# Kernel optimization log

Measured on AMD Instinct MI355X. Metric: run time of the kernel, lower is better.

Reference implementation:

```python
import jax, jax.numpy as jnp
import numpy as np

DEPTH = 5

def _gru_step(h, fmess, bgraph, W_z_w, W_z_b, W_r_w, U_r_w, U_r_b, W_h_w, W_h_b):
    # h: [E, H]; gather neighbor states -> [E, K, H]
    h_nei = h[bgraph]
    sum_h = h_nei.sum(axis=1)                                   # [E, H]
    z_in = jnp.concatenate([fmess, sum_h], axis=1)              # [E, I+H]
    z = jax.nn.sigmoid(z_in @ W_z_w.T + W_z_b)                  # [E, H]
    r1 = (fmess @ W_r_w.T)[:, None, :]                          # [E, 1, H]
    r2 = jnp.einsum('ekh,oh->eko', h_nei, U_r_w) + U_r_b        # [E, K, H]
    r = jax.nn.sigmoid(r1 + r2)
    sum_gated_h = (r * h_nei).sum(axis=1)                       # [E, H]
    h_in = jnp.concatenate([fmess, sum_gated_h], axis=1)
    pre_h = jnp.tanh(h_in @ W_h_w.T + W_h_b)
    new_h = (1.0 - z) * sum_h + z * pre_h
    # row 0 is the padding message; zero it each step
    return new_h.at[0, :].set(0.0)


def setup_inputs() -> dict:
    key = jax.random.key(0)
    ks = jax.random.split(key, 8)
    E, K, I, H = 150000, 8, 128, 128
    s = 0.05
    return {
        'fmess': jax.random.normal(ks[0], (E, I), dtype=jnp.float32),
        'bgraph': jax.random.randint(ks[1], (E, K), 0, E, dtype=jnp.int64),
        'W_z_w': jax.random.normal(ks[2], (H, I + H), dtype=jnp.float32) * s,
        'W_z_b': jnp.zeros((H,), dtype=jnp.float32),
        'W_r_w': jax.random.normal(ks[3], (H, I), dtype=jnp.float32) * s,
        'U_r_w': jax.random.normal(ks[4], (H, H), dtype=jnp.float32) * s,
        'U_r_b': jnp.zeros((H,), dtype=jnp.float32),
        'W_h_w': jax.random.normal(ks[5], (H, I + H), dtype=jnp.float32) * s,
        'W_h_b': jnp.zeros((H,), dtype=jnp.float32),
    }


def reference(fmess, bgraph, W_z_w, W_z_b, W_r_w, U_r_w, U_r_b, W_h_w, W_h_b):
    E = fmess.shape[0]
    H = W_z_w.shape[0]
    h = jnp.zeros((E, H), dtype=fmess.dtype)
    for _ in range(DEPTH):
        h = _gru_step(h, fmess, bgraph, W_z_w, W_z_b, W_r_w, U_r_w, U_r_b, W_h_w, W_h_b)
    return h
```

## Files before the change

kernel.cpp:

```cpp
#include <hip/hip_runtime.h>
#include <cstddef>
#include <cstdint>

typedef __attribute__((ext_vector_type(8))) short bf16x8;
typedef __attribute__((ext_vector_type(4))) float f32x4;
typedef __attribute__((ext_vector_type(2))) float f32x2;
typedef unsigned int u32t;
typedef unsigned short u16t;
typedef unsigned char u8t;

__device__ inline u16t f2bf(float f) {
  union { float f; unsigned u; } c; c.f = f;
  return (u16t)((c.u + 0x7FFFu + ((c.u >> 16) & 1u)) >> 16);
}
__device__ inline float ubits(u32t u) { union { u32t u; float f; } c; c.u = u; return c.f; }
__device__ inline float bf2f(u16t u) { return ubits(((u32t)u) << 16); }
__device__ inline float fsig(float x) { return __builtin_amdgcn_rcpf(1.f + __expf(-x)); }
__device__ inline float ftanh(float x) {
  float t = __expf(-2.f * fabsf(x));
  return copysignf((1.f - t) * __builtin_amdgcn_rcpf(1.f + t), x);
}
__device__ inline u32t f32x4_to_fp8(float a, float b, float c, float d) {
  int v = __builtin_amdgcn_cvt_pk_fp8_f32(a, b, 0, false);
  v = __builtin_amdgcn_cvt_pk_fp8_f32(c, d, v, true);
  return (u32t)v;
}

__global__ __launch_bounds__(256) void conv_weights(
    const float* __restrict__ Wz, const float* __restrict__ Wr,
    const float* __restrict__ Ur, const float* __restrict__ Wh,
    short* __restrict__ out)
{
  int i = blockIdx.x * 256 + threadIdx.x;
  if (i >= 6 * 16384) return;
  int mat = i >> 14, idx = i & 16383;
  int o = idx >> 7, c = idx & 127;
  float v = 0.f;
  switch (mat) {
    case 0: v = Wz[o * 256 + c];        break;
    case 1: v = Wz[o * 256 + 128 + c];  break;
    case 2: v = Wr[o * 128 + c];        break;
    case 3: v = Wh[o * 256 + c];        break;
    case 4: v = Wh[o * 256 + 128 + c];  break;
    case 5: v = Ur[o * 128 + c];        break;
  }
  out[i] = (short)f2bf(v);
}

__global__ __launch_bounds__(256) void conv_fmess(const float* __restrict__ src,
                                                  u16t* __restrict__ dst, size_t n8)
{
  size_t i = (size_t)blockIdx.x * 256 + threadIdx.x;
  if (i >= n8) return;
  const float4 a = *reinterpret_cast<const float4*>(src + i * 8);
  const float4 b = *reinterpret_cast<const float4*>(src + i * 8 + 4);
  uint4 o;
  o.x = ((u32t)f2bf(a.y) << 16) | f2bf(a.x);
  o.y = ((u32t)f2bf(a.w) << 16) | f2bf(a.z);
  o.z = ((u32t)f2bf(b.y) << 16) | f2bf(b.x);
  o.w = ((u32t)f2bf(b.w) << 16) | f2bf(b.z);
  *reinterpret_cast<uint4*>(dst + i * 8) = o;
}

__global__ void detect64(const int* __restrict__ bg, int* __restrict__ flag) {
  int t = threadIdx.x;
  int v = bg[2 * t + 1];
  unsigned long long m = __ballot(v == 0);
  if (t == 0) *flag = (m == ~0ull) ? 1 : 0;
}

__global__ __launch_bounds__(256) void compact_bg(const int* __restrict__ bg,
                                                  const int* __restrict__ flag,
                                                  int* __restrict__ bg32, int n)
{
  int i = blockIdx.x * 256 + threadIdx.x;
  if (i < n) bg32[i] = (*flag) ? bg[2 * (size_t)i] : bg[i];
}

#define GLD(H0, H1, H2, H3, P0, P1, P2, P3, q, nbb) { \
  int i0_ = __shfl(idx_all, (hf * 4 + (q)) * 8 + (nbb) + 0); \
  int i1_ = __shfl(idx_all, (hf * 4 + (q)) * 8 + (nbb) + 1); \
  int i2_ = __shfl(idx_all, (hf * 4 + (q)) * 8 + (nbb) + 2); \
  int i3_ = __shfl(idx_all, (hf * 4 + (q)) * 8 + (nbb) + 3); \
  H0 = *reinterpret_cast<const uint2*>(Hin + (size_t)i0_ * 128 + l5 * 4); \
  H1 = *reinterpret_cast<const uint2*>(Hin + (size_t)i1_ * 128 + l5 * 4); \
  H2 = *reinterpret_cast<const uint2*>(Hin + (size_t)i2_ * 128 + l5 * 4); \
  H3 = *reinterpret_cast<const uint2*>(Hin + (size_t)i3_ * 128 + l5 * 4); \
  P0 = *reinterpret_cast<const u32t*>(Pin + (size_t)i0_ * 128 + l5 * 4); \
  P1 = *reinterpret_cast<const u32t*>(Pin + (size_t)i1_ * 128 + l5 * 4); \
  P2 = *reinterpret_cast<const u32t*>(Pin + (size_t)i2_ * 128 + l5 * 4); \
  P3 = *reinterpret_cast<const u32t*>(Pin + (size_t)i3_ * 128 + l5 * 4); \
}

#define PRN(HV, PW) { \
  f32x2 plo_ = __builtin_amdgcn_cvt_pk_f32_fp8((int)(PW), false); \
  f32x2 phi_ = __builtin_amdgcn_cvt_pk_f32_fp8((int)(PW), true); \
  float h0_ = ubits(HV.x << 16), h1_ = ubits(HV.x & 0xffff0000u); \
  float h2_ = ubits(HV.y << 16), h3_ = ubits(HV.y & 0xffff0000u); \
  s0 += h0_; g0 += fsig(r10 + plo_.x) * h0_; \
  s1 += h1_; g1 += fsig(r11 + plo_.y) * h1_; \
  s2 += h2_; g2 += fsig(r12 + phi_.x) * h2_; \
  s3 += h3_; g3 += fsig(r13 + phi_.y) * h3_; \
}

#define PR4(HH0, HH1, HH2, HH3, PP0, PP1, PP2, PP3) \
  PRN(HH0, PP0) PRN(HH1, PP1) PRN(HH2, PP2) PRN(HH3, PP3)

#define INITR(q) { \
  int rl_ = wave * 8 + hf * 4 + (q); \
  uint2 rp_ = *reinterpret_cast<const uint2*>(s_R1 + rl_ * 136 + l5 * 4); \
  r10 = ubits(rp_.x << 16); r11 = ubits(rp_.x & 0xffff0000u); \
  r12 = ubits(rp_.y << 16); r13 = ubits(rp_.y & 0xffff0000u); \
  s0 = s1 = s2 = s3 = 0.f; g0 = g1 = g2 = g3 = 0.f; \
}

#define FINR(q) { \
  int rl_ = wave * 8 + hf * 4 + (q); \
  uint2 sp_, gp_; \
  sp_.x = ((u32t)f2bf(s1) << 16) | f2bf(s0); \
  sp_.y = ((u32t)f2bf(s3) << 16) | f2bf(s2); \
  gp_.x = ((u32t)f2bf(g1) << 16) | f2bf(g0); \
  gp_.y = ((u32t)f2bf(g3) << 16) | f2bf(g2); \
  *reinterpret_cast<uint2*>(s_sb + rl_ * 136 + l5 * 4) = sp_; \
  *reinterpret_cast<uint2*>(s_gb + rl_ * 136 + l5 * 4) = gp_; \
}

template<int MODE>
__global__ __launch_bounds__(512, 4) void step_k(
    const u16t* __restrict__ fmb,
    const int*  __restrict__ bg32,
    const u16t* __restrict__ Hin,
    const u8t*  __restrict__ Pin,
    const short* __restrict__ wbf,
    const float* __restrict__ bz, const float* __restrict__ urb, const float* __restrict__ bh,
    u16t* __restrict__ Hout, u8t* __restrict__ Pout, float* __restrict__ houtf, int E)
{
  __shared__ __align__(16) char smem[52224];
  u16t* s_R1 = (u16t*)smem;
  u16t* s_sb = (u16t*)(smem + 17408);
  u16t* s_gb = (u16t*)(smem + 34816);

  const int tid = threadIdx.x, wave = tid >> 6, lane = tid & 63;
  const int cl = lane & 15, kg = lane >> 4;
  const int l5 = lane & 31, hf = lane >> 5;
  const int base = blockIdx.x * 64;
  const int wrow = (wave & 1) * 32, ncol = (wave >> 1) * 32;

  const short* Wzf = wbf;
  const short* Wzh = wbf + 16384;
  const short* Wr  = wbf + 2 * 16384;
  const short* Whf = wbf + 3 * 16384;
  const short* Whh = wbf + 4 * 16384;
  const short* Ur  = wbf + 5 * 16384;

  bf16x8 af[2][4];
  #pragma unroll
  for (int rt = 0; rt < 2; ++rt) {
    int ar = base + wrow + rt * 16 + cl;
    if (ar >= E) ar = E - 1;
    #pragma unroll
    for (int ks = 0; ks < 4; ++ks)
      af[rt][ks] = *reinterpret_cast<const bf16x8*>(fmb + (size_t)ar * 128 + ks * 32 + kg * 8);
  }

  int idx_all = 0;
  if (MODE != 0) {
    int er = base + wave * 8 + (lane >> 3);
    if (er >= E) er = 0;
    idx_all = bg32[(size_t)er * 8 + (lane & 7)];
  }

  if (MODE != 0) {
    f32x4 racc[2][2];
    #pragma unroll
    for (int rt = 0; rt < 2; ++rt)
      #pragma unroll
      for (int nt = 0; nt < 2; ++nt) racc[rt][nt] = (f32x4){0.f, 0.f, 0.f, 0.f};
    #pragma unroll
    for (int ks = 0; ks < 4; ++ks) {
      #pragma unroll
      for (int nt = 0; nt < 2; ++nt) {
        bf16x8 b = *reinterpret_cast<const bf16x8*>(Wr + (size_t)(ncol + nt * 16 + cl) * 128 + ks * 32 + kg * 8);
        #pragma unroll
        for (int rt = 0; rt < 2; ++rt)
          racc[rt][nt] = __builtin_amdgcn_mfma_f32_16x16x32_bf16(af[rt][ks], b, racc[rt][nt], 0, 0, 0);
      }
    }
    #pragma unroll
    for (int nt = 0; nt < 2; ++nt) {
      int n = ncol + nt * 16 + cl;
      float bias = urb[n];
      #pragma unroll
      for (int rt = 0; rt < 2; ++rt)
        #pragma unroll
        for (int r = 0; r < 4; ++r)
          s_R1[(wrow + rt * 16 + kg * 4 + r) * 136 + n] = f2bf(racc[rt][nt][r] + bias);
    }
    __syncthreads();

    uint2 HA0, HA1, HA2, HA3, HB0, HB1, HB2, HB3;
    u32t  PA0, PA1, PA2, PA3, PB0, PB1, PB2, PB3;
    float s0, s1, s2, s3, g0, g1, g2, g3, r10, r11, r12, r13;

    GLD(HA0, HA1, HA2, HA3, PA0, PA1, PA2, PA3, 0, 0)
    GLD(HB0, HB1, HB2, HB3, PB0, PB1, PB2, PB3, 0, 4)
    INITR(0)
    PR4(HA0, HA1, HA2, HA3, PA0, PA1, PA2, PA3)
    GLD(HA0, HA1, HA2, HA3, PA0, PA1, PA2, PA3, 1, 0)
    PR4(HB0, HB1, HB2, HB3, PB0, PB1, PB2, PB3)
    FINR(0)
    GLD(HB0, HB1, HB2, HB3, PB0, PB1, PB2, PB3, 1, 4)
    INITR(1)
    PR4(HA0, HA1, HA2, HA3, PA0, PA1, PA2, PA3)
    GLD(HA0, HA1, HA2, HA3, PA0, PA1, PA2, PA3, 2, 0)
    PR4(HB0, HB1, HB2, HB3, PB0, PB1, PB2, PB3)
    FINR(1)
    GLD(HB0, HB1, HB2, HB3, PB0, PB1, PB2, PB3, 2, 4)
    INITR(2)
    PR4(HA0, HA1, HA2, HA3, PA0, PA1, PA2, PA3)
    GLD(HA0, HA1, HA2, HA3, PA0, PA1, PA2, PA3, 3, 0)
    PR4(HB0, HB1, HB2, HB3, PB0, PB1, PB2, PB3)
    FINR(2)
    GLD(HB0, HB1, HB2, HB3, PB0, PB1, PB2, PB3, 3, 4)
    INITR(3)
    PR4(HA0, HA1, HA2, HA3, PA0, PA1, PA2, PA3)
    PR4(HB0, HB1, HB2, HB3, PB0, PB1, PB2, PB3)
    FINR(3)
    __syncthreads();
  }

  {
    f32x4 acc[2][2];
    #pragma unroll
    for (int rt = 0; rt < 2; ++rt)
      #pragma unroll
      for (int nt = 0; nt < 2; ++nt) acc[rt][nt] = (f32x4){0.f, 0.f, 0.f, 0.f};
    #pragma unroll
    for (int ks = 0; ks < 4; ++ks) {
      bf16x8 as0, as1;
      if (MODE != 0) {
        as0 = *reinterpret_cast<const bf16x8*>(s_sb + (wrow + cl) * 136 + ks * 32 + kg * 8);
        as1 = *reinterpret_cast<const bf16x8*>(s_sb + (wrow + 16 + cl) * 136 + ks * 32 + kg * 8);
      }
      #pragma unroll
      for (int nt = 0; nt < 2; ++nt) {
        int n = ncol + nt * 16 + cl;
        bf16x8 b1 = *reinterpret_cast<const bf16x8*>(Wzf + (size_t)n * 128 + ks * 32 + kg * 8);
        acc[0][nt] = __builtin_amdgcn_mfma_f32_16x16x32_bf16(af[0][ks], b1, acc[0][nt], 0, 0, 0);
        acc[1][nt] = __builtin_amdgcn_mfma_f32_16x16x32_bf16(af[1][ks], b1, acc[1][nt], 0, 0, 0);
        if (MODE != 0) {
          bf16x8 b2 = *reinterpret_cast<const bf16x8*>(Wzh + (size_t)n * 128 + ks * 32 + kg * 8);
          acc[0][nt] = __builtin_amdgcn_mfma_f32_16x16x32_bf16(as0, b2, acc[0][nt], 0, 0, 0);
          acc[1][nt] = __builtin_amdgcn_mfma_f32_16x16x32_bf16(as1, b2, acc[1][nt], 0, 0, 0);
        }
      }
    }
    #pragma unroll
    for (int nt = 0; nt < 2; ++nt) {
      int n = ncol + nt * 16 + cl;
      float bzv = bz[n];
      #pragma unroll
      for (int rt = 0; rt < 2; ++rt)
        #pragma unroll
        for (int r = 0; r < 4; ++r)
          s_R1[(wrow + rt * 16 + kg * 4 + r) * 136 + n] = f2bf(fsig(acc[rt][nt][r] + bzv));
    }
  }

  float nh_sv[2][2][4];
  {
    f32x4 acc[2][2];
    #pragma unroll
    for (int rt = 0; rt < 2; ++rt)
      #pragma unroll
      for (int nt = 0; nt < 2; ++nt) acc[rt][nt] = (f32x4){0.f, 0.f, 0.f, 0.f};
    #pragma unroll
    for (int ks = 0; ks < 4; ++ks) {
      bf16x8 ag0, ag1;
      if (MODE != 0) {
        ag0 = *reinterpret_cast<const bf16x8*>(s_gb + (wrow + cl) * 136 + ks * 32 + kg * 8);
        ag1 = *reinterpret_cast<const bf16x8*>(s_gb + (wrow + 16 + cl) * 136 + ks * 32 + kg * 8);
      }
      #pragma unroll
      for (int nt = 0; nt < 2; ++nt) {
        int n = ncol + nt * 16 + cl;
        bf16x8 b1 = *reinterpret_cast<const bf16x8*>(Whf + (size_t)n * 128 + ks * 32 + kg * 8);
        acc[0][nt] = __builtin_amdgcn_mfma_f32_16x16x32_bf16(af[0][ks], b1, acc[0][nt], 0, 0, 0);
        acc[1][nt] = __builtin_amdgcn_mfma_f32_16x16x32_bf16(af[1][ks], b1, acc[1][nt], 0, 0, 0);
        if (MODE != 0) {
          bf16x8 b2 = *reinterpret_cast<const bf16x8*>(Whh + (size_t)n * 128 + ks * 32 + kg * 8);
          acc[0][nt] = __builtin_amdgcn_mfma_f32_16x16x32_bf16(ag0, b2, acc[0][nt], 0, 0, 0);
          acc[1][nt] = __builtin_amdgcn_mfma_f32_16x16x32_bf16(ag1, b2, acc[1][nt], 0, 0, 0);
        }
      }
    }
    #pragma unroll
    for (int nt = 0; nt < 2; ++nt) {
      int n = ncol + nt * 16 + cl;
      float bhv = bh[n];
      #pragma unroll
      for (int rt = 0; rt < 2; ++rt)
        #pragma unroll
        for (int r = 0; r < 4; ++r) {
          int rowt = wrow + rt * 16 + kg * 4 + r;
          int e = base + rowt;
          float pre = ftanh(acc[rt][nt][r] + bhv);
          float z   = bf2f(s_R1[rowt * 136 + n]);
          float sh  = (MODE == 0) ? 0.f : bf2f(s_sb[rowt * 136 + n]);
          float nh  = (1.f - z) * sh + z * pre;
          if (e == 0) nh = 0.f;
          nh_sv[rt][nt][r] = nh;
        }
    }
  }

  if (MODE == 2) {
    __syncthreads();
    float* so = (float*)(smem + 17408);
    #pragma unroll
    for (int nt = 0; nt < 2; ++nt) {
      int n = ncol + nt * 16 + cl;
      #pragma unroll
      for (int rt = 0; rt < 2; ++rt)
        #pragma unroll
        for (int r = 0; r < 4; ++r)
          so[(wrow + rt * 16 + kg * 4 + r) * 132 + n] = nh_sv[rt][nt][r];
    }
    __syncthreads();
    #pragma unroll
    for (int it = 0; it < 4; ++it) {
      int slot = it * 512 + tid;
      int row = slot >> 5, seg = slot & 31;
      if (base + row < E)
        *reinterpret_cast<float4*>(houtf + (size_t)(base + row) * 128 + seg * 4) =
            *reinterpret_cast<const float4*>(so + row * 132 + seg * 4);
    }
  } else {
    __syncthreads();
    #pragma unroll
    for (int nt = 0; nt < 2; ++nt) {
      int n = ncol + nt * 16 + cl;
      #pragma unroll
      for (int rt = 0; rt < 2; ++rt)
        #pragma unroll
        for (int r = 0; r < 4; ++r)
          s_sb[(wrow + rt * 16 + kg * 4 + r) * 136 + n] = f2bf(nh_sv[rt][nt][r]);
    }
    __syncthreads();
    f32x4 pacc[2][2];
    #pragma unroll
    for (int rt = 0; rt < 2; ++rt)
      #pragma unroll
      for (int nt = 0; nt < 2; ++nt) pacc[rt][nt] = (f32x4){0.f, 0.f, 0.f, 0.f};
    #pragma unroll
    for (int ks = 0; ks < 4; ++ks) {
      bf16x8 ah0 = *reinterpret_cast<const bf16x8*>(s_sb + (wrow + cl) * 136 + ks * 32 + kg * 8);
      bf16x8 ah1 = *reinterpret_cast<const bf16x8*>(s_sb + (wrow + 16 + cl) * 136 + ks * 32 + kg * 8);
      #pragma unroll
      for (int nt = 0; nt < 2; ++nt) {
        bf16x8 b = *reinterpret_cast<const bf16x8*>(Ur + (size_t)(ncol + nt * 16 + cl) * 128 + ks * 32 + kg * 8);
        pacc[0][nt] = __builtin_amdgcn_mfma_f32_16x16x32_bf16(ah0, b, pacc[0][nt], 0, 0, 0);
        pacc[1][nt] = __builtin_amdgcn_mfma_f32_16x16x32_bf16(ah1, b, pacc[1][nt], 0, 0, 0);
      }
    }
    #pragma unroll
    for (int nt = 0; nt < 2; ++nt) {
      int n = ncol + nt * 16 + cl;
      #pragma unroll
      for (int rt = 0; rt < 2; ++rt)
        #pragma unroll
        for (int r = 0; r < 4; ++r)
          s_gb[(wrow + rt * 16 + kg * 4 + r) * 136 + n] = f2bf(pacc[rt][nt][r]);
    }
    __syncthreads();
    #pragma unroll
    for (int it = 0; it < 2; ++it) {
      int slot = it * 512 + tid;
      int row = slot >> 4, seg = slot & 15;
      if (base + row < E)
        *reinterpret_cast<uint4*>(Hout + (size_t)(base + row) * 128 + seg * 8) =
            *reinterpret_cast<const uint4*>(s_sb + row * 136 + seg * 8);
    }
    #pragma unroll
    for (int it = 0; it < 4; ++it) {
      int slot = it * 512 + tid;
      int row = slot >> 5, cg = slot & 31;
      if (base + row < E) {
        uint2 pv = *reinterpret_cast<const uint2*>(s_gb + row * 136 + cg * 4);
        float p0 = ubits(pv.x << 16), p1 = ubits(pv.x & 0xffff0000u);
        float p2 = ubits(pv.y << 16), p3 = ubits(pv.y & 0xffff0000u);
        *reinterpret_cast<u32t*>(Pout + (size_t)(base + row) * 128 + cg * 4) =
            f32x4_to_fp8(p0, p1, p2, p3);
      }
    }
  }
}

extern "C" void kernel_launch(void* const* d_in, const int* in_sizes, int n_in,
                              void* d_out, int out_size, void* d_ws, size_t ws_size,
                              hipStream_t stream) {
  const float* fmess = (const float*)d_in[0];
  const int*   bg    = (const int*)d_in[1];
  const float* Wz    = (const float*)d_in[2];
  const float* bz    = (const float*)d_in[3];
  const float* Wrw   = (const float*)d_in[4];
  const float* Urw   = (const float*)d_in[5];
  const float* urb   = (const float*)d_in[6];
  const float* Wh    = (const float*)d_in[7];
  const float* bh    = (const float*)d_in[8];
  float* out = (float*)d_out;

  const int E = in_sizes[0] / 128;
  const size_t EH = (size_t)E * 128;
  const size_t wshorts = 6 * 16384;

  u16t* HA   = (u16t*)d_ws;
  u8t*  PA   = (u8t*)(HA + EH);
  u16t* fmb  = (u16t*)(PA + EH);
  int*  bg32 = (int*)(fmb + EH);
  short* wbf = (short*)(bg32 + (size_t)E * 8);
  int*  flag = (int*)(wbf + wshorts);
  u16t* HB = (u16t*)d_out;
  u8t*  PB = (u8t*)(HB + EH);

  conv_weights<<<384, 256, 0, stream>>>(Wz, Wrw, Urw, Wh, wbf);
  detect64<<<1, 64, 0, stream>>>(bg, flag);
  compact_bg<<<(E * 8 + 255) / 256, 256, 0, stream>>>(bg, flag, bg32, E * 8);
  conv_fmess<<<(int)((EH / 8 + 255) / 256), 256, 0, stream>>>(fmess, fmb, EH / 8);

  const int grid = (E + 63) / 64;
  step_k<0><<<grid, 512, 0, stream>>>(fmb, bg32, nullptr, nullptr, wbf, bz, urb, bh, HB, PB, nullptr, E);
  step_k<1><<<grid, 512, 0, stream>>>(fmb, bg32, HB, PB, wbf, bz, urb, bh, HA, PA, nullptr, E);
  step_k<1><<<grid, 512, 0, stream>>>(fmb, bg32, HA, PA, wbf, bz, urb, bh, HB, PB, nullptr, E);
  step_k<1><<<grid, 512, 0, stream>>>(fmb, bg32, HB, PB, wbf, bz, urb, bh, HA, PA, nullptr, E);
  step_k<2><<<grid, 512, 0, stream>>>(fmb, bg32, HA, PA, wbf, bz, urb, bh, nullptr, nullptr, out, E);
}
```

Before: 777.2 us.

## Interleave H and P rows into one buffer and shrink shared memory

Stores the bf16 hidden state and the fp8 projected state side by side in a single 384-byte row per edge. Each gathered neighbour then touches one contiguous region instead of two separate arrays. The pre-activation (h) GEMM is moved ahead of the z GEMM, so the tanh result can reuse the gated-sum LDS buffer and z is applied straight from registers. This cuts shared memory from 52KB to 34KB, which may allow more resident blocks, at the cost of an extra barrier.

```diff
diff --git a/kernel.cpp b/kernel.cpp
--- a/kernel.cpp
+++ b/kernel.cpp
@@ -82,14 +82,18 @@
   int i1_ = __shfl(idx_all, (hf * 4 + (q)) * 8 + (nbb) + 1); \
   int i2_ = __shfl(idx_all, (hf * 4 + (q)) * 8 + (nbb) + 2); \
   int i3_ = __shfl(idx_all, (hf * 4 + (q)) * 8 + (nbb) + 3); \
-  H0 = *reinterpret_cast<const uint2*>(Hin + (size_t)i0_ * 128 + l5 * 4); \
-  H1 = *reinterpret_cast<const uint2*>(Hin + (size_t)i1_ * 128 + l5 * 4); \
-  H2 = *reinterpret_cast<const uint2*>(Hin + (size_t)i2_ * 128 + l5 * 4); \
-  H3 = *reinterpret_cast<const uint2*>(Hin + (size_t)i3_ * 128 + l5 * 4); \
-  P0 = *reinterpret_cast<const u32t*>(Pin + (size_t)i0_ * 128 + l5 * 4); \
-  P1 = *reinterpret_cast<const u32t*>(Pin + (size_t)i1_ * 128 + l5 * 4); \
-  P2 = *reinterpret_cast<const u32t*>(Pin + (size_t)i2_ * 128 + l5 * 4); \
-  P3 = *reinterpret_cast<const u32t*>(Pin + (size_t)i3_ * 128 + l5 * 4); \
+  const u16t* r0_ = HPin + (size_t)i0_ * 192; \
+  const u16t* r1_ = HPin + (size_t)i1_ * 192; \
+  const u16t* r2_ = HPin + (size_t)i2_ * 192; \
+  const u16t* r3_ = HPin + (size_t)i3_ * 192; \
+  H0 = *reinterpret_cast<const uint2*>(r0_ + l5 * 4); \
+  H1 = *reinterpret_cast<const uint2*>(r1_ + l5 * 4); \
+  H2 = *reinterpret_cast<const uint2*>(r2_ + l5 * 4); \
+  H3 = *reinterpret_cast<const uint2*>(r3_ + l5 * 4); \
+  P0 = *reinterpret_cast<const u32t*>(r0_ + 128 + l5 * 2); \
+  P1 = *reinterpret_cast<const u32t*>(r1_ + 128 + l5 * 2); \
+  P2 = *reinterpret_cast<const u32t*>(r2_ + 128 + l5 * 2); \
+  P3 = *reinterpret_cast<const u32t*>(r3_ + 128 + l5 * 2); \
 }
 
 #define PRN(HV, PW) { \
@@ -129,16 +133,15 @@
 __global__ __launch_bounds__(512, 4) void step_k(
     const u16t* __restrict__ fmb,
     const int*  __restrict__ bg32,
-    const u16t* __restrict__ Hin,
-    const u8t*  __restrict__ Pin,
+    const u16t* __restrict__ HPin,
     const short* __restrict__ wbf,
     const float* __restrict__ bz, const float* __restrict__ urb, const float* __restrict__ bh,
-    u16t* __restrict__ Hout, u8t* __restrict__ Pout, float* __restrict__ houtf, int E)
+    u16t* __restrict__ HPout, float* __restrict__ houtf, int E)
 {
-  __shared__ __align__(16) char smem[52224];
+  __shared__ __align__(16) char smem[34816];
   u16t* s_R1 = (u16t*)smem;
+  u16t* s_gb = (u16t*)smem;
   u16t* s_sb = (u16t*)(smem + 17408);
-  u16t* s_gb = (u16t*)(smem + 34816);
 
   const int tid = threadIdx.x, wave = tid >> 6, lane = tid & 63;
   const int cl = lane & 15, kg = lane >> 4;
@@ -237,6 +240,46 @@
       for (int nt = 0; nt < 2; ++nt) acc[rt][nt] = (f32x4){0.f, 0.f, 0.f, 0.f};
     #pragma unroll
     for (int ks = 0; ks < 4; ++ks) {
+      bf16x8 ag0, ag1;
+      if (MODE != 0) {
+        ag0 = *reinterpret_cast<const bf16x8*>(s_gb + (wrow + cl) * 136 + ks * 32 + kg * 8);
+        ag1 = *reinterpret_cast<const bf16x8*>(s_gb + (wrow + 16 + cl) * 136 + ks * 32 + kg * 8);
+      }
+      #pragma unroll
+      for (int nt = 0; nt < 2; ++nt) {
+        int n = ncol + nt * 16 + cl;
+        bf16x8 b1 = *reinterpret_cast<const bf16x8*>(Whf + (size_t)n * 128 + ks * 32 + kg * 8);
+        acc[0][nt] = __builtin_amdgcn_mfma_f32_16x16x32_bf16(af[0][ks], b1, acc[0][nt], 0, 0, 0);
+        acc[1][nt] = __builtin_amdgcn_mfma_f32_16x16x32_bf16(af[1][ks], b1, acc[1][nt], 0, 0, 0);
+        if (MODE != 0) {
+          bf16x8 b2 = *reinterpret_cast<const bf16x8*>(Whh + (size_t)n * 128 + ks * 32 + kg * 8);
+          acc[0][nt] = __builtin_amdgcn_mfma_f32_16x16x32_bf16(ag0, b2, acc[0][nt], 0, 0, 0);
+          acc[1][nt] = __builtin_amdgcn_mfma_f32_16x16x32_bf16(ag1, b2, acc[1][nt], 0, 0, 0);
+        }
+      }
+    }
+    __syncthreads();
+    #pragma unroll
+    for (int nt = 0; nt < 2; ++nt) {
+      int n = ncol + nt * 16 + cl;
+      float bhv = bh[n];
+      #pragma unroll
+      for (int rt = 0; rt < 2; ++rt)
+        #pragma unroll
+        for (int r = 0; r < 4; ++r)
+          s_gb[(wrow + rt * 16 + kg * 4 + r) * 136 + n] = f2bf(ftanh(acc[rt][nt][r] + bhv));
+    }
+  }
+
+  float nh_sv[2][2][4];
+  {
+    f32x4 acc[2][2];
+    #pragma unroll
+    for (int rt = 0; rt < 2; ++rt)
+      #pragma unroll
+      for (int nt = 0; nt < 2; ++nt) acc[rt][nt] = (f32x4){0.f, 0.f, 0.f, 0.f};
+    #pragma unroll
+    for (int ks = 0; ks < 4; ++ks) {
       bf16x8 as0, as1;
       if (MODE != 0) {
         as0 = *reinterpret_cast<const bf16x8*>(s_sb + (wrow + cl) * 136 + ks * 32 + kg * 8);
@@ -262,50 +305,11 @@
       #pragma unroll
       for (int rt = 0; rt < 2; ++rt)
         #pragma unroll
-        for (int r = 0; r < 4; ++r)
-          s_R1[(wrow + rt * 16 + kg * 4 + r) * 136 + n] = f2bf(fsig(acc[rt][nt][r] + bzv));
-    }
-  }
-
-  float nh_sv[2][2][4];
-  {
-    f32x4 acc[2][2];
-    #pragma unroll
-    for (int rt = 0; rt < 2; ++rt)
-      #pragma unroll
-      for (int nt = 0; nt < 2; ++nt) acc[rt][nt] = (f32x4){0.f, 0.f, 0.f, 0.f};
-    #pragma unroll
-    for (int ks = 0; ks < 4; ++ks) {
-      bf16x8 ag0, ag1;
-      if (MODE != 0) {
-        ag0 = *reinterpret_cast<const bf16x8*>(s_gb + (wrow + cl) * 136 + ks * 32 + kg * 8);
-        ag1 = *reinterpret_cast<const bf16x8*>(s_gb + (wrow + 16 + cl) * 136 + ks * 32 + kg * 8);
-      }
-      #pragma unroll
-      for (int nt = 0; nt < 2; ++nt) {
-        int n = ncol + nt * 16 + cl;
-        bf16x8 b1 = *reinterpret_cast<const bf16x8*>(Whf + (size_t)n * 128 + ks * 32 + kg * 8);
-        acc[0][nt] = __builtin_amdgcn_mfma_f32_16x16x32_bf16(af[0][ks], b1, acc[0][nt], 0, 0, 0);
-        acc[1][nt] = __builtin_amdgcn_mfma_f32_16x16x32_bf16(af[1][ks], b1, acc[1][nt], 0, 0, 0);
-        if (MODE != 0) {
-          bf16x8 b2 = *reinterpret_cast<const bf16x8*>(Whh + (size_t)n * 128 + ks * 32 + kg * 8);
-          acc[0][nt] = __builtin_amdgcn_mfma_f32_16x16x32_bf16(ag0, b2, acc[0][nt], 0, 0, 0);
-          acc[1][nt] = __builtin_amdgcn_mfma_f32_16x16x32_bf16(ag1, b2, acc[1][nt], 0, 0, 0);
-        }
-      }
-    }
-    #pragma unroll
-    for (int nt = 0; nt < 2; ++nt) {
-      int n = ncol + nt * 16 + cl;
-      float bhv = bh[n];
-      #pragma unroll
-      for (int rt = 0; rt < 2; ++rt)
-        #pragma unroll
         for (int r = 0; r < 4; ++r) {
           int rowt = wrow + rt * 16 + kg * 4 + r;
           int e = base + rowt;
-          float pre = ftanh(acc[rt][nt][r] + bhv);
-          float z   = bf2f(s_R1[rowt * 136 + n]);
+          float z   = fsig(acc[rt][nt][r] + bzv);
+          float pre = bf2f(s_gb[rowt * 136 + n]);
           float sh  = (MODE == 0) ? 0.f : bf2f(s_sb[rowt * 136 + n]);
           float nh  = (1.f - z) * sh + z * pre;
           if (e == 0) nh = 0.f;
@@ -313,10 +317,10 @@
         }
     }
   }
+  __syncthreads();
 
   if (MODE == 2) {
-    __syncthreads();
-    float* so = (float*)(smem + 17408);
+    float* so = (float*)smem;
     #pragma unroll
     for (int nt = 0; nt < 2; ++nt) {
       int n = ncol + nt * 16 + cl;
@@ -336,7 +340,6 @@
             *reinterpret_cast<const float4*>(so + row * 132 + seg * 4);
     }
   } else {
-    __syncthreads();
     #pragma unroll
     for (int nt = 0; nt < 2; ++nt) {
       int n = ncol + nt * 16 + cl;
@@ -378,7 +381,7 @@
       int slot = it * 512 + tid;
       int row = slot >> 4, seg = slot & 15;
       if (base + row < E)
-        *reinterpret_cast<uint4*>(Hout + (size_t)(base + row) * 128 + seg * 8) =
+        *reinterpret_cast<uint4*>(HPout + (size_t)(base + row) * 192 + seg * 8) =
             *reinterpret_cast<const uint4*>(s_sb + row * 136 + seg * 8);
     }
     #pragma unroll
@@ -389,7 +392,7 @@
         uint2 pv = *reinterpret_cast<const uint2*>(s_gb + row * 136 + cg * 4);
         float p0 = ubits(pv.x << 16), p1 = ubits(pv.x & 0xffff0000u);
         float p2 = ubits(pv.y << 16), p3 = ubits(pv.y & 0xffff0000u);
-        *reinterpret_cast<u32t*>(Pout + (size_t)(base + row) * 128 + cg * 4) =
+        *reinterpret_cast<u32t*>(HPout + (size_t)(base + row) * 192 + 128 + cg * 2) =
             f32x4_to_fp8(p0, p1, p2, p3);
       }
     }
@@ -414,14 +417,12 @@
   const size_t EH = (size_t)E * 128;
   const size_t wshorts = 6 * 16384;
 
-  u16t* HA   = (u16t*)d_ws;
-  u8t*  PA   = (u8t*)(HA + EH);
-  u16t* fmb  = (u16t*)(PA + EH);
+  u16t* HPA  = (u16t*)d_ws;
+  u16t* fmb  = HPA + (size_t)E * 192;
   int*  bg32 = (int*)(fmb + EH);
   short* wbf = (short*)(bg32 + (size_t)E * 8);
   int*  flag = (int*)(wbf + wshorts);
-  u16t* HB = (u16t*)d_out;
-  u8t*  PB = (u8t*)(HB + EH);
+  u16t* HPB = (u16t*)d_out;
 
   conv_weights<<<384, 256, 0, stream>>>(Wz, Wrw, Urw, Wh, wbf);
   detect64<<<1, 64, 0, stream>>>(bg, flag);
@@ -429,9 +430,9 @@
   conv_fmess<<<(int)((EH / 8 + 255) / 256), 256, 0, stream>>>(fmess, fmb, EH / 8);
 
   const int grid = (E + 63) / 64;
-  step_k<0><<<grid, 512, 0, stream>>>(fmb, bg32, nullptr, nullptr, wbf, bz, urb, bh, HB, PB, nullptr, E);
-  step_k<1><<<grid, 512, 0, stream>>>(fmb, bg32, HB, PB, wbf, bz, urb, bh, HA, PA, nullptr, E);
-  step_k<1><<<grid, 512, 0, stream>>>(fmb, bg32, HA, PA, wbf, bz, urb, bh, HB, PB, nullptr, E);
-  step_k<1><<<grid, 512, 0, stream>>>(fmb, bg32, HB, PB, wbf, bz, urb, bh, HA, PA, nullptr, E);
-  step_k<2><<<grid, 512, 0, stream>>>(fmb, bg32, HA, PA, wbf, bz, urb, bh, nullptr, nullptr, out, E);
-}
+  step_k<0><<<grid, 512, 0, stream>>>(fmb, bg32, nullptr, wbf, bz, urb, bh, HPB, nullptr, E);
+  step_k<1><<<grid, 512, 0, stream>>>(fmb, bg32, HPB, wbf, bz, urb, bh, HPA, nullptr, E);
+  step_k<1><<<grid, 512, 0, stream>>>(fmb, bg32, HPA, wbf, bz, urb, bh, HPB, nullptr, E);
+  step_k<1><<<grid, 512, 0, stream>>>(fmb, bg32, HPB, wbf, bz, urb, bh, HPA, nullptr, E);
+  step_k<2><<<grid, 512, 0, stream>>>(fmb, bg32, HPA, wbf, bz, urb, bh, nullptr, out, E);
+}
```

Result: no change. 784.4 us (+0.9%).

## Compute U_r projection per gathered neighbor instead of storing fp8 P per row

Applied to the files above, without the earlier changes.

Drops the precomputed per-row U_r·h projection (stored as fp8 P alongside H) and instead gathers full bf16 neighbor rows into shared memory. It then runs MFMA on each gathered tile to compute U_r·h_nei on the fly, double-buffering the next chunk's gathers. This removes the extra P write and P gathers per step and the trailing Ur GEMM, but adds 8x more Ur MFMA work, more shared memory (lower occupancy) and extra barriers. The z/h GEMM order is also reshuffled to reuse shared buffers.

```diff
diff --git a/kernel.cpp b/kernel.cpp
--- a/kernel.cpp
+++ b/kernel.cpp
@@ -4,10 +4,8 @@
 
 typedef __attribute__((ext_vector_type(8))) short bf16x8;
 typedef __attribute__((ext_vector_type(4))) float f32x4;
-typedef __attribute__((ext_vector_type(2))) float f32x2;
 typedef unsigned int u32t;
 typedef unsigned short u16t;
-typedef unsigned char u8t;
 
 __device__ inline u16t f2bf(float f) {
   union { float f; unsigned u; } c; c.f = f;
@@ -19,11 +17,6 @@
 __device__ inline float ftanh(float x) {
   float t = __expf(-2.f * fabsf(x));
   return copysignf((1.f - t) * __builtin_amdgcn_rcpf(1.f + t), x);
-}
-__device__ inline u32t f32x4_to_fp8(float a, float b, float c, float d) {
-  int v = __builtin_amdgcn_cvt_pk_fp8_f32(a, b, 0, false);
-  v = __builtin_amdgcn_cvt_pk_fp8_f32(c, d, v, true);
-  return (u32t)v;
 }
 
 __global__ __launch_bounds__(256) void conv_weights(
@@ -77,52 +70,61 @@
   if (i < n) bg32[i] = (*flag) ? bg[2 * (size_t)i] : bg[i];
 }
 
-#define GLD(H0, H1, H2, H3, P0, P1, P2, P3, q, nbb) { \
-  int i0_ = __shfl(idx_all, (hf * 4 + (q)) * 8 + (nbb) + 0); \
-  int i1_ = __shfl(idx_all, (hf * 4 + (q)) * 8 + (nbb) + 1); \
-  int i2_ = __shfl(idx_all, (hf * 4 + (q)) * 8 + (nbb) + 2); \
-  int i3_ = __shfl(idx_all, (hf * 4 + (q)) * 8 + (nbb) + 3); \
-  H0 = *reinterpret_cast<const uint2*>(Hin + (size_t)i0_ * 128 + l5 * 4); \
-  H1 = *reinterpret_cast<const uint2*>(Hin + (size_t)i1_ * 128 + l5 * 4); \
-  H2 = *reinterpret_cast<const uint2*>(Hin + (size_t)i2_ * 128 + l5 * 4); \
-  H3 = *reinterpret_cast<const uint2*>(Hin + (size_t)i3_ * 128 + l5 * 4); \
-  P0 = *reinterpret_cast<const u32t*>(Pin + (size_t)i0_ * 128 + l5 * 4); \
-  P1 = *reinterpret_cast<const u32t*>(Pin + (size_t)i1_ * 128 + l5 * 4); \
-  P2 = *reinterpret_cast<const u32t*>(Pin + (size_t)i2_ * 128 + l5 * 4); \
-  P3 = *reinterpret_cast<const u32t*>(Pin + (size_t)i3_ * 128 + l5 * 4); \
-}
-
-#define PRN(HV, PW) { \
-  f32x2 plo_ = __builtin_amdgcn_cvt_pk_f32_fp8((int)(PW), false); \
-  f32x2 phi_ = __builtin_amdgcn_cvt_pk_f32_fp8((int)(PW), true); \
-  float h0_ = ubits(HV.x << 16), h1_ = ubits(HV.x & 0xffff0000u); \
-  float h2_ = ubits(HV.y << 16), h3_ = ubits(HV.y & 0xffff0000u); \
-  s0 += h0_; g0 += fsig(r10 + plo_.x) * h0_; \
-  s1 += h1_; g1 += fsig(r11 + plo_.y) * h1_; \
-  s2 += h2_; g2 += fsig(r12 + phi_.x) * h2_; \
-  s3 += h3_; g3 += fsig(r13 + phi_.y) * h3_; \
-}
-
-#define PR4(HH0, HH1, HH2, HH3, PP0, PP1, PP2, PP3) \
-  PRN(HH0, PP0) PRN(HH1, PP1) PRN(HH2, PP2) PRN(HH3, PP3)
-
-#define INITR(q) { \
-  int rl_ = wave * 8 + hf * 4 + (q); \
-  uint2 rp_ = *reinterpret_cast<const uint2*>(s_R1 + rl_ * 136 + l5 * 4); \
-  r10 = ubits(rp_.x << 16); r11 = ubits(rp_.x & 0xffff0000u); \
-  r12 = ubits(rp_.y << 16); r13 = ubits(rp_.y & 0xffff0000u); \
-  s0 = s1 = s2 = s3 = 0.f; g0 = g1 = g2 = g3 = 0.f; \
-}
-
-#define FINR(q) { \
-  int rl_ = wave * 8 + hf * 4 + (q); \
-  uint2 sp_, gp_; \
-  sp_.x = ((u32t)f2bf(s1) << 16) | f2bf(s0); \
-  sp_.y = ((u32t)f2bf(s3) << 16) | f2bf(s2); \
-  gp_.x = ((u32t)f2bf(g1) << 16) | f2bf(g0); \
-  gp_.y = ((u32t)f2bf(g3) << 16) | f2bf(g2); \
-  *reinterpret_cast<uint2*>(s_sb + rl_ * 136 + l5 * 4) = sp_; \
-  *reinterpret_cast<uint2*>(s_gb + rl_ * 136 + l5 * 4) = gp_; \
+#define ANLOAD(D0, D1, D2, D3, c) { \
+  const u16t* rp_ = Hin + (size_t)idxs[c] * 128 + kg * 8; \
+  D0 = *reinterpret_cast<const uint4*>(rp_); \
+  D1 = *reinterpret_cast<const uint4*>(rp_ + 32); \
+  D2 = *reinterpret_cast<const uint4*>(rp_ + 64); \
+  D3 = *reinterpret_cast<const uint4*>(rp_ + 96); \
+}
+
+#define CHUNK(c, A0, A1, A2, A3, B0, B1, B2, B3, LAST) { \
+  __syncthreads();   \
+  { int slot_ = cg * 16 + cl; \
+    *reinterpret_cast<uint4*>(htg + slot_ * 140 + 0  + kg * 8) = A0; \
+    *reinterpret_cast<uint4*>(htg + slot_ * 140 + 32 + kg * 8) = A1; \
+    *reinterpret_cast<uint4*>(htg + slot_ * 140 + 64 + kg * 8) = A2; \
+    *reinterpret_cast<uint4*>(htg + slot_ * 140 + 96 + kg * 8) = A3; } \
+  if (!(LAST)) { ANLOAD(B0, B1, B2, B3, (c) + 1) } \
+  __syncthreads();   \
+  f32x4 pac[4][2]; \
+  _Pragma("unroll") for (int t = 0; t < 4; ++t) { \
+    pac[t][0] = (f32x4){0.f, 0.f, 0.f, 0.f}; pac[t][1] = (f32x4){0.f, 0.f, 0.f, 0.f}; } \
+  _Pragma("unroll") for (int ks = 0; ks < 4; ++ks) { \
+    bf16x8 w0_ = *reinterpret_cast<const bf16x8*>(Ur + (size_t)(ncol + cl) * 128 + ks * 32 + kg * 8); \
+    bf16x8 w1_ = *reinterpret_cast<const bf16x8*>(Ur + (size_t)(ncol + 16 + cl) * 128 + ks * 32 + kg * 8); \
+    bf16x8 a0_ = *reinterpret_cast<const bf16x8*>(htg + (0 * 16 + cl) * 140 + ks * 32 + kg * 8); \
+    bf16x8 a1_ = *reinterpret_cast<const bf16x8*>(htg + (1 * 16 + cl) * 140 + ks * 32 + kg * 8); \
+    bf16x8 a2_ = *reinterpret_cast<const bf16x8*>(htg + (2 * 16 + cl) * 140 + ks * 32 + kg * 8); \
+    bf16x8 a3_ = *reinterpret_cast<const bf16x8*>(htg + (3 * 16 + cl) * 140 + ks * 32 + kg * 8); \
+    pac[0][0] = __builtin_amdgcn_mfma_f32_16x16x32_bf16(a0_, w0_, pac[0][0], 0, 0, 0); \
+    pac[0][1] = __builtin_amdgcn_mfma_f32_16x16x32_bf16(a0_, w1_, pac[0][1], 0, 0, 0); \
+    pac[1][0] = __builtin_amdgcn_mfma_f32_16x16x32_bf16(a1_, w0_, pac[1][0], 0, 0, 0); \
+    pac[1][1] = __builtin_amdgcn_mfma_f32_16x16x32_bf16(a1_, w1_, pac[1][1], 0, 0, 0); \
+    pac[2][0] = __builtin_amdgcn_mfma_f32_16x16x32_bf16(a2_, w0_, pac[2][0], 0, 0, 0); \
+    pac[2][1] = __builtin_amdgcn_mfma_f32_16x16x32_bf16(a2_, w1_, pac[2][1], 0, 0, 0); \
+    pac[3][0] = __builtin_amdgcn_mfma_f32_16x16x32_bf16(a3_, w0_, pac[3][0], 0, 0, 0); \
+    pac[3][1] = __builtin_amdgcn_mfma_f32_16x16x32_bf16(a3_, w1_, pac[3][1], 0, 0, 0); \
+  } \
+  _Pragma("unroll") for (int t = 0; t < 4; ++t) { \
+    int erow_ = g * 32 + (c) * 8 + t * 2 + (kg >> 1); \
+    _Pragma("unroll") for (int ct = 0; ct < 2; ++ct) { \
+      int col_ = ncol + ct * 16 + cl; \
+      float r1_ = bf2f(s_R1[erow_ * 136 + col_]); \
+      float sh_ = 0.f, sg_ = 0.f; \
+      _Pragma("unroll") for (int r = 0; r < 4; ++r) { \
+        float hv_ = bf2f(htg[(t * 16 + kg * 4 + r) * 140 + col_]); \
+        sh_ += hv_; \
+        sg_ += fsig(r1_ + pac[t][ct][r]) * hv_; \
+      } \
+      sh_ += __shfl_xor(sh_, 16); \
+      sg_ += __shfl_xor(sg_, 16); \
+      if ((kg & 1) == 0) { \
+        s_sb[erow_ * 136 + col_] = f2bf(sh_); \
+        s_gb[erow_ * 136 + col_] = f2bf(sg_); \
+      } \
+    } \
+  } \
 }
 
 template<int MODE>
@@ -130,21 +132,22 @@
     const u16t* __restrict__ fmb,
     const int*  __restrict__ bg32,
     const u16t* __restrict__ Hin,
-    const u8t*  __restrict__ Pin,
     const short* __restrict__ wbf,
     const float* __restrict__ bz, const float* __restrict__ urb, const float* __restrict__ bh,
-    u16t* __restrict__ Hout, u8t* __restrict__ Pout, float* __restrict__ houtf, int E)
+    u16t* __restrict__ Hout, float* __restrict__ houtf, int E)
 {
-  __shared__ __align__(16) char smem[52224];
-  u16t* s_R1 = (u16t*)smem;
-  u16t* s_sb = (u16t*)(smem + 17408);
-  u16t* s_gb = (u16t*)(smem + 34816);
+  __shared__ __align__(16) char smem[70656];
+  u16t* s_R1  = (u16t*)smem;
+  u16t* s_gb  = (u16t*)smem;
+  u16t* s_sb  = (u16t*)(smem + 17408);
+  u16t* htile = (u16t*)(smem + 34816);
 
   const int tid = threadIdx.x, wave = tid >> 6, lane = tid & 63;
   const int cl = lane & 15, kg = lane >> 4;
-  const int l5 = lane & 31, hf = lane >> 5;
   const int base = blockIdx.x * 64;
-  const int wrow = (wave & 1) * 32, ncol = (wave >> 1) * 32;
+  const int g = wave & 1, cg = wave >> 1;
+  const int wrow = g * 32, ncol = cg * 32;
+  u16t* htg = htile + g * (64 * 140);
 
   const short* Wzf = wbf;
   const short* Wzh = wbf + 16384;
@@ -153,6 +156,59 @@
   const short* Whh = wbf + 4 * 16384;
   const short* Ur  = wbf + 5 * 16384;
 
+  if (MODE != 0) {
+    {
+      bf16x8 af0[2][4];
+      #pragma unroll
+      for (int rt = 0; rt < 2; ++rt) {
+        int ar = base + wrow + rt * 16 + cl;
+        if (ar >= E) ar = E - 1;
+        #pragma unroll
+        for (int ks = 0; ks < 4; ++ks)
+          af0[rt][ks] = *reinterpret_cast<const bf16x8*>(fmb + (size_t)ar * 128 + ks * 32 + kg * 8);
+      }
+      f32x4 racc[2][2];
+      #pragma unroll
+      for (int rt = 0; rt < 2; ++rt)
+        #pragma unroll
+        for (int nt = 0; nt < 2; ++nt) racc[rt][nt] = (f32x4){0.f, 0.f, 0.f, 0.f};
+      #pragma unroll
+      for (int ks = 0; ks < 4; ++ks) {
+        #pragma unroll
+        for (int nt = 0; nt < 2; ++nt) {
+          bf16x8 b = *reinterpret_cast<const bf16x8*>(Wr + (size_t)(ncol + nt * 16 + cl) * 128 + ks * 32 + kg * 8);
+          racc[0][nt] = __builtin_amdgcn_mfma_f32_16x16x32_bf16(af0[0][ks], b, racc[0][nt], 0, 0, 0);
+          racc[1][nt] = __builtin_amdgcn_mfma_f32_16x16x32_bf16(af0[1][ks], b, racc[1][nt], 0, 0, 0);
+        }
+      }
+      #pragma unroll
+      for (int nt = 0; nt < 2; ++nt) {
+        int n = ncol + nt * 16 + cl;
+        float bias = urb[n];
+        #pragma unroll
+        for (int rt = 0; rt < 2; ++rt)
+          #pragma unroll
+          for (int r = 0; r < 4; ++r)
+            s_R1[(wrow + rt * 16 + kg * 4 + r) * 136 + n] = f2bf(racc[rt][nt][r] + bias);
+      }
+    }
+
+    int idxs[4];
+    #pragma unroll
+    for (int c = 0; c < 4; ++c) {
+      int e_g = base + g * 32 + c * 8 + cg * 2 + (cl >> 3);
+      if (e_g >= E) e_g = 0;
+      idxs[c] = bg32[(size_t)e_g * 8 + (cl & 7)];
+    }
+    uint4 A0, A1, A2, A3, B0, B1, B2, B3;
+    ANLOAD(A0, A1, A2, A3, 0)
+    CHUNK(0, A0, A1, A2, A3, B0, B1, B2, B3, 0)
+    CHUNK(1, B0, B1, B2, B3, A0, A1, A2, A3, 0)
+    CHUNK(2, A0, A1, A2, A3, B0, B1, B2, B3, 0)
+    CHUNK(3, B0, B1, B2, B3, A0, A1, A2, A3, 1)
+    __syncthreads();
+  }
+
   bf16x8 af[2][4];
   #pragma unroll
   for (int rt = 0; rt < 2; ++rt) {
@@ -163,72 +219,46 @@
       af[rt][ks] = *reinterpret_cast<const bf16x8*>(fmb + (size_t)ar * 128 + ks * 32 + kg * 8);
   }
 
-  int idx_all = 0;
-  if (MODE != 0) {
-    int er = base + wave * 8 + (lane >> 3);
-    if (er >= E) er = 0;
-    idx_all = bg32[(size_t)er * 8 + (lane & 7)];
-  }
-
-  if (MODE != 0) {
-    f32x4 racc[2][2];
+  {
+    f32x4 acc[2][2];
     #pragma unroll
     for (int rt = 0; rt < 2; ++rt)
       #pragma unroll
-      for (int nt = 0; nt < 2; ++nt) racc[rt][nt] = (f32x4){0.f, 0.f, 0.f, 0.f};
+      for (int nt = 0; nt < 2; ++nt) acc[rt][nt] = (f32x4){0.f, 0.f, 0.f, 0.f};
     #pragma unroll
     for (int ks = 0; ks < 4; ++ks) {
+      bf16x8 ag0, ag1;
+      if (MODE != 0) {
+        ag0 = *reinterpret_cast<const bf16x8*>(s_gb + (wrow + cl) * 136 + ks * 32 + kg * 8);
+        ag1 = *reinterpret_cast<const bf16x8*>(s_gb + (wrow + 16 + cl) * 136 + ks * 32 + kg * 8);
+      }
       #pragma unroll
       for (int nt = 0; nt < 2; ++nt) {
-        bf16x8 b = *reinterpret_cast<const bf16x8*>(Wr + (size_t)(ncol + nt * 16 + cl) * 128 + ks * 32 + kg * 8);
-        #pragma unroll
-        for (int rt = 0; rt < 2; ++rt)
-          racc[rt][nt] = __builtin_amdgcn_mfma_f32_16x16x32_bf16(af[rt][ks], b, racc[rt][nt], 0, 0, 0);
-      }
-    }
+        int n = ncol + nt * 16 + cl;
+        bf16x8 b1 = *reinterpret_cast<const bf16x8*>(Whf + (size_t)n * 128 + ks * 32 + kg * 8);
+        acc[0][nt] = __builtin_amdgcn_mfma_f32_16x16x32_bf16(af[0][ks], b1, acc[0][nt], 0, 0, 0);
+        acc[1][nt] = __builtin_amdgcn_mfma_f32_16x16x32_bf16(af[1][ks], b1, acc[1][nt], 0, 0, 0);
+        if (MODE != 0) {
+          bf16x8 b2 = *reinterpret_cast<const bf16x8*>(Whh + (size_t)n * 128 + ks * 32 + kg * 8);
+          acc[0][nt] = __builtin_amdgcn_mfma_f32_16x16x32_bf16(ag0, b2, acc[0][nt], 0, 0, 0);
+          acc[1][nt] = __builtin_amdgcn_mfma_f32_16x16x32_bf16(ag1, b2, acc[1][nt], 0, 0, 0);
+        }
+      }
+    }
+    __syncthreads();
     #pragma unroll
     for (int nt = 0; nt < 2; ++nt) {
       int n = ncol + nt * 16 + cl;
-      float bias = urb[n];
+      float bhv = bh[n];
       #pragma unroll
       for (int rt = 0; rt < 2; ++rt)
         #pragma unroll
         for (int r = 0; r < 4; ++r)
-          s_R1[(wrow + rt * 16 + kg * 4 + r) * 136 + n] = f2bf(racc[rt][nt][r] + bias);
-    }
-    __syncthreads();
-
-    uint2 HA0, HA1, HA2, HA3, HB0, HB1, HB2, HB3;
-    u32t  PA0, PA1, PA2, PA3, PB0, PB1, PB2, PB3;
-    float s0, s1, s2, s3, g0, g1, g2, g3, r10, r11, r12, r13;
-
-    GLD(HA0, HA1, HA2, HA3, PA0, PA1, PA2, PA3, 0, 0)
-    GLD(HB0, HB1, HB2, HB3, PB0, PB1, PB2, PB3, 0, 4)
-    INITR(0)
-    PR4(HA0, HA1, HA2, HA3, PA0, PA1, PA2, PA3)
-    GLD(HA0, HA1, HA2, HA3, PA0, PA1, PA2, PA3, 1, 0)
-    PR4(HB0, HB1, HB2, HB3, PB0, PB1, PB2, PB3)
-    FINR(0)
-    GLD(HB0, HB1, HB2, HB3, PB0, PB1, PB2, PB3, 1, 4)
-    INITR(1)
-    PR4(HA0, HA1, HA2, HA3, PA0, PA1, PA2, PA3)
-    GLD(HA0, HA1, HA2, HA3, PA0, PA1, PA2, PA3, 2, 0)
-    PR4(HB0, HB1, HB2, HB3, PB0, PB1, PB2, PB3)
-    FINR(1)
-    GLD(HB0, HB1, HB2, HB3, PB0, PB1, PB2, PB3, 2, 4)
-    INITR(2)
-    PR4(HA0, HA1, HA2, HA3, PA0, PA1, PA2, PA3)
-    GLD(HA0, HA1, HA2, HA3, PA0, PA1, PA2, PA3, 3, 0)
-    PR4(HB0, HB1, HB2, HB3, PB0, PB1, PB2, PB3)
-    FINR(2)
-    GLD(HB0, HB1, HB2, HB3, PB0, PB1, PB2, PB3, 3, 4)
-    INITR(3)
-    PR4(HA0, HA1, HA2, HA3, PA0, PA1, PA2, PA3)
-    PR4(HB0, HB1, HB2, HB3, PB0, PB1, PB2, PB3)
-    FINR(3)
-    __syncthreads();
-  }
-
+          s_gb[(wrow + rt * 16 + kg * 4 + r) * 136 + n] = f2bf(ftanh(acc[rt][nt][r] + bhv));
+    }
+  }
+
+  float nh_sv[2][2][4];
   {
     f32x4 acc[2][2];
     #pragma unroll
@@ -262,50 +292,11 @@
       #pragma unroll
       for (int rt = 0; rt < 2; ++rt)
         #pragma unroll
-        for (int r = 0; r < 4; ++r)
-          s_R1[(wrow + rt * 16 + kg * 4 + r) * 136 + n] = f2bf(fsig(acc[rt][nt][r] + bzv));
-    }
-  }
-
-  float nh_sv[2][2][4];
-  {
-    f32x4 acc[2][2];
-    #pragma unroll
-    for (int rt = 0; rt < 2; ++rt)
-      #pragma unroll
-      for (int nt = 0; nt < 2; ++nt) acc[rt][nt] = (f32x4){0.f, 0.f, 0.f, 0.f};
-    #pragma unroll
-    for (int ks = 0; ks < 4; ++ks) {
-      bf16x8 ag0, ag1;
-      if (MODE != 0) {
-        ag0 = *reinterpret_cast<const bf16x8*>(s_gb + (wrow + cl) * 136 + ks * 32 + kg * 8);
-        ag1 = *reinterpret_cast<const bf16x8*>(s_gb + (wrow + 16 + cl) * 136 + ks * 32 + kg * 8);
-      }
-      #pragma unroll
-      for (int nt = 0; nt < 2; ++nt) {
-        int n = ncol + nt * 16 + cl;
-        bf16x8 b1 = *reinterpret_cast<const bf16x8*>(Whf + (size_t)n * 128 + ks * 32 + kg * 8);
-        acc[0][nt] = __builtin_amdgcn_mfma_f32_16x16x32_bf16(af[0][ks], b1, acc[0][nt], 0, 0, 0);
-        acc[1][nt] = __builtin_amdgcn_mfma_f32_16x16x32_bf16(af[1][ks], b1, acc[1][nt], 0, 0, 0);
-        if (MODE != 0) {
-          bf16x8 b2 = *reinterpret_cast<const bf16x8*>(Whh + (size_t)n * 128 + ks * 32 + kg * 8);
-          acc[0][nt] = __builtin_amdgcn_mfma_f32_16x16x32_bf16(ag0, b2, acc[0][nt], 0, 0, 0);
-          acc[1][nt] = __builtin_amdgcn_mfma_f32_16x16x32_bf16(ag1, b2, acc[1][nt], 0, 0, 0);
-        }
-      }
-    }
-    #pragma unroll
-    for (int nt = 0; nt < 2; ++nt) {
-      int n = ncol + nt * 16 + cl;
-      float bhv = bh[n];
-      #pragma unroll
-      for (int rt = 0; rt < 2; ++rt)
-        #pragma unroll
         for (int r = 0; r < 4; ++r) {
           int rowt = wrow + rt * 16 + kg * 4 + r;
           int e = base + rowt;
-          float pre = ftanh(acc[rt][nt][r] + bhv);
-          float z   = bf2f(s_R1[rowt * 136 + n]);
+          float z   = fsig(acc[rt][nt][r] + bzv);
+          float pre = bf2f(s_gb[rowt * 136 + n]);
           float sh  = (MODE == 0) ? 0.f : bf2f(s_sb[rowt * 136 + n]);
           float nh  = (1.f - z) * sh + z * pre;
           if (e == 0) nh = 0.f;
@@ -313,10 +304,10 @@
         }
     }
   }
+  __syncthreads();
 
   if (MODE == 2) {
-    __syncthreads();
-    float* so = (float*)(smem + 17408);
+    float* so = (float*)(smem + 34816);
     #pragma unroll
     for (int nt = 0; nt < 2; ++nt) {
       int n = ncol + nt * 16 + cl;
@@ -336,7 +327,7 @@
             *reinterpret_cast<const float4*>(so + row * 132 + seg * 4);
     }
   } else {
-    __syncthreads();
+    u16t* so = (u16t*)(smem + 34816);
     #pragma unroll
     for (int nt = 0; nt < 2; ++nt) {
       int n = ncol + nt * 16 + cl;
@@ -344,33 +335,7 @@
       for (int rt = 0; rt < 2; ++rt)
         #pragma unroll
         for (int r = 0; r < 4; ++r)
-          s_sb[(wrow + rt * 16 + kg * 4 + r) * 136 + n] = f2bf(nh_sv[rt][nt][r]);
-    }
-    __syncthreads();
-    f32x4 pacc[2][2];
-    #pragma unroll
-    for (int rt = 0; rt < 2; ++rt)
-      #pragma unroll
-      for (int nt = 0; nt < 2; ++nt) pacc[rt][nt] = (f32x4){0.f, 0.f, 0.f, 0.f};
-    #pragma unroll
-    for (int ks = 0; ks < 4; ++ks) {
-      bf16x8 ah0 = *reinterpret_cast<const bf16x8*>(s_sb + (wrow + cl) * 136 + ks * 32 + kg * 8);
-      bf16x8 ah1 = *reinterpret_cast<const bf16x8*>(s_sb + (wrow + 16 + cl) * 136 + ks * 32 + kg * 8);
-      #pragma unroll
-      for (int nt = 0; nt < 2; ++nt) {
-        bf16x8 b = *reinterpret_cast<const bf16x8*>(Ur + (size_t)(ncol + nt * 16 + cl) * 128 + ks * 32 + kg * 8);
-        pacc[0][nt] = __builtin_amdgcn_mfma_f32_16x16x32_bf16(ah0, b, pacc[0][nt], 0, 0, 0);
-        pacc[1][nt] = __builtin_amdgcn_mfma_f32_16x16x32_bf16(ah1, b, pacc[1][nt], 0, 0, 0);
-      }
-    }
-    #pragma unroll
-    for (int nt = 0; nt < 2; ++nt) {
-      int n = ncol + nt * 16 + cl;
-      #pragma unroll
-      for (int rt = 0; rt < 2; ++rt)
-        #pragma unroll
-        for (int r = 0; r < 4; ++r)
-          s_gb[(wrow + rt * 16 + kg * 4 + r) * 136 + n] = f2bf(pacc[rt][nt][r]);
+          so[(wrow + rt * 16 + kg * 4 + r) * 128 + n] = f2bf(nh_sv[rt][nt][r]);
     }
     __syncthreads();
     #pragma unroll
@@ -379,19 +344,7 @@
       int row = slot >> 4, seg = slot & 15;
       if (base + row < E)
         *reinterpret_cast<uint4*>(Hout + (size_t)(base + row) * 128 + seg * 8) =
-            *reinterpret_cast<const uint4*>(s_sb + row * 136 + seg * 8);
-    }
-    #pragma unroll
-    for (int it = 0; it < 4; ++it) {
-      int slot = it * 512 + tid;
-      int row = slot >> 5, cg = slot & 31;
-      if (base + row < E) {
-        uint2 pv = *reinterpret_cast<const uint2*>(s_gb + row * 136 + cg * 4);
-        float p0 = ubits(pv.x << 16), p1 = ubits(pv.x & 0xffff0000u);
-        float p2 = ubits(pv.y << 16), p3 = ubits(pv.y & 0xffff0000u);
-        *reinterpret_cast<u32t*>(Pout + (size_t)(base + row) * 128 + cg * 4) =
-            f32x4_to_fp8(p0, p1, p2, p3);
-      }
+            *reinterpret_cast<const uint4*>(so + row * 128 + seg * 8);
     }
   }
 }
@@ -415,13 +368,11 @@
   const size_t wshorts = 6 * 16384;
 
   u16t* HA   = (u16t*)d_ws;
-  u8t*  PA   = (u8t*)(HA + EH);
-  u16t* fmb  = (u16t*)(PA + EH);
+  u16t* fmb  = HA + EH;
   int*  bg32 = (int*)(fmb + EH);
   short* wbf = (short*)(bg32 + (size_t)E * 8);
   int*  flag = (int*)(wbf + wshorts);
   u16t* HB = (u16t*)d_out;
-  u8t*  PB = (u8t*)(HB + EH);
 
   conv_weights<<<384, 256, 0, stream>>>(Wz, Wrw, Urw, Wh, wbf);
   detect64<<<1, 64, 0, stream>>>(bg, flag);
@@ -429,9 +380,9 @@
   conv_fmess<<<(int)((EH / 8 + 255) / 256), 256, 0, stream>>>(fmess, fmb, EH / 8);
 
   const int grid = (E + 63) / 64;
-  step_k<0><<<grid, 512, 0, stream>>>(fmb, bg32, nullptr, nullptr, wbf, bz, urb, bh, HB, PB, nullptr, E);
-  step_k<1><<<grid, 512, 0, stream>>>(fmb, bg32, HB, PB, wbf, bz, urb, bh, HA, PA, nullptr, E);
-  step_k<1><<<grid, 512, 0, stream>>>(fmb, bg32, HA, PA, wbf, bz, urb, bh, HB, PB, nullptr, E);
-  step_k<1><<<grid, 512, 0, stream>>>(fmb, bg32, HB, PB, wbf, bz, urb, bh, HA, PA, nullptr, E);
-  step_k<2><<<grid, 512, 0, stream>>>(fmb, bg32, HA, PA, wbf, bz, urb, bh, nullptr, nullptr, out, E);
-}
+  step_k<0><<<grid, 512, 0, stream>>>(fmb, bg32, nullptr, wbf, bz, urb, bh, HB, nullptr, E);
+  step_k<1><<<grid, 512, 0, stream>>>(fmb, bg32, HB, wbf, bz, urb, bh, HA, nullptr, E);
+  step_k<1><<<grid, 512, 0, stream>>>(fmb, bg32, HA, wbf, bz, urb, bh, HB, nullptr, E);
+  step_k<1><<<grid, 512, 0, stream>>>(fmb, bg32, HB, wbf, bz, urb, bh, HA, nullptr, E);
+  step_k<2><<<grid, 512, 0, stream>>>(fmb, bg32, HA, wbf, bz, urb, bh, nullptr, out, E);
+}
```

New measurement: 1.277 ms. +64.3%, slower.
